# Performance work log

Measured on AMD Instinct MI355X. Metric: run time of the kernel, lower is better.

## Reference

```python
import jax, jax.numpy as jnp
from jax import lax
import numpy as np

B, N, C = 16, 4096, 64
RATIO = 0.25
M = int(N * RATIO)      # 1024 sampled centers
R = 0.2                 # radius
K = 64                  # max_num_neighbors
H = 128                 # MLP hidden/out width
NEG = -1e30


def setup_inputs() -> dict:
    key = jax.random.key(0)
    k1, k2, k3, k4 = jax.random.split(key, 4)
    pos = jax.random.uniform(k1, (B, N, 3), dtype=jnp.float32)
    x = jax.random.normal(k2, (B, N, C), dtype=jnp.float32)
    W1 = jax.random.normal(k3, (C + 3, H), dtype=jnp.float32) / np.sqrt(C + 3)
    b1 = jnp.zeros((H,), jnp.float32)
    W2 = jax.random.normal(k4, (H, H), dtype=jnp.float32) / np.sqrt(H)
    b2 = jnp.zeros((H,), jnp.float32)
    return {"x": x, "pos": pos, "W1": W1, "b1": b1, "W2": W2, "b2": b2}


def _fps_single(p, m):
    """Farthest point sampling on one cloud p:[N,3] -> m int32 indices (start at 0)."""
    n = p.shape[0]
    big = jnp.full((n,), jnp.finfo(p.dtype).max, dtype=p.dtype)

    def step(carry, _):
        dists, last = carry
        d = jnp.sum((p - p[last]) ** 2, axis=-1)       # [N]
        dists = jnp.minimum(dists, d)
        nxt = jnp.argmax(dists).astype(jnp.int32)
        return (dists, nxt), nxt

    (_, _), idxs = lax.scan(step, (big, jnp.int32(0)), None, length=m - 1)
    return jnp.concatenate([jnp.zeros((1,), jnp.int32), idxs])


def reference(x, pos, W1, b1, W2, b2):
    # --- FPS: sample M centers per cloud ---
    idx = jax.vmap(lambda p: _fps_single(p, M))(pos)                 # [B,M] int32
    pos_s = jax.vmap(lambda p, i: p[i])(pos, idx)                    # [B,M,3]

    # --- radius ball query: pairwise sq-dists via |a|^2+|b|^2-2ab (no [B,M,N,3]) ---
    pn = jnp.sum(pos * pos, axis=-1)                                 # [B,N]
    sn = jnp.sum(pos_s * pos_s, axis=-1)                             # [B,M]
    d2 = sn[:, :, None] + pn[:, None, :] - 2.0 * jnp.einsum("bmc,bnc->bmn", pos_s, pos)
    mask = d2 <= R * R                                               # [B,M,N]

    # first K in-radius neighbors by index (torch_cluster-style capped neighbor list)
    ar = jnp.arange(N, dtype=jnp.int32)
    scored = jnp.where(mask, -ar[None, None, :], -N)                 # valid -> -idx
    vals, _ = lax.top_k(scored, K)                                   # [B,M,K]
    nbr = -vals                                                      # neighbor indices, N = invalid
    valid = nbr < N                                                  # [B,M,K]
    nbr_c = jnp.minimum(nbr, N - 1)

    # --- gather -> MLP -> masked max aggregation (PointConv, aggr='max') ---
    x_j = jax.vmap(lambda xb, ib: xb[ib])(x, nbr_c)                  # [B,M,K,C]
    pos_j = jax.vmap(lambda pb, ib: pb[ib])(pos, nbr_c)              # [B,M,K,3]
    feat = jnp.concatenate([x_j, pos_j - pos_s[:, :, None, :]], axis=-1)  # [B,M,K,C+3]

    h = jax.nn.relu(jnp.einsum("bmkc,ch->bmkh", feat, W1) + b1)
    h = jax.nn.relu(jnp.einsum("bmkh,hg->bmkg", h, W2) + b2)          # [B,M,K,H]

    h = jnp.where(valid[..., None], h, NEG)
    out = jnp.max(h, axis=2)                                          # [B,M,H]
    out = jnp.where(jnp.any(valid, axis=2)[..., None], out, 0.0)
    return out, pos_s
```

## Files before the change

kernel.cpp:

```cpp
#include <hip/hip_runtime.h>
#include <cstdint>
#include <cstddef>

#define BB 16
#define NN 4096
#define CC 64
#define MM 1024
#define KK 64
#define HH 128
#define NEGV -1.0e30f

#define FTH 256
#define FPT 16
#define NPROD 16
#define GTOT 256
#define PSTRIDE 32

#define KC1 96
#define SA 104
#define SH 136
#define HSTRIDE 41984

typedef __attribute__((ext_vector_type(8))) short bf16x8;
typedef __attribute__((ext_vector_type(4))) float f32x4;
typedef __attribute__((ext_vector_type(2))) float f32x2;

__device__ __forceinline__ unsigned int f2bf(float f) {
  unsigned int u = __float_as_uint(f);
  return (u + 0x7fffu + ((u >> 16) & 1u)) >> 16;
}
__device__ __forceinline__ void split2(float f, unsigned int& h, unsigned int& l) {
  h = f2bf(f);
  float hf = __uint_as_float(h << 16);
  l = f2bf(f - hf);
}

template <int CTRL, int RM>
__device__ __forceinline__ void dpp_max64(unsigned int& hi, unsigned int& lo) {
  unsigned int shi = (unsigned int)__builtin_amdgcn_update_dpp(
      (int)hi, (int)hi, CTRL, RM, 0xf, false);
  unsigned int slo = (unsigned int)__builtin_amdgcn_update_dpp(
      (int)lo, (int)lo, CTRL, RM, 0xf, false);
  unsigned long long cur = ((unsigned long long)hi << 32) | lo;
  unsigned long long oth = ((unsigned long long)shi << 32) | slo;
  if (oth > cur) { hi = shi; lo = slo; }
}

__global__ __launch_bounds__(256) void pn_kernel(const float* __restrict__ pos,
                                                 float* __restrict__ pn) {
#pragma clang fp contract(off)
  int i = blockIdx.x * 256 + threadIdx.x;
  if (i < BB * NN) {
    float x = pos[(size_t)i * 3 + 0];
    float y = pos[(size_t)i * 3 + 1];
    float z = pos[(size_t)i * 3 + 2];
    pn[i] = (x * x + y * y) + z * z;
  }
}

__global__ __launch_bounds__(128) void wprep_kernel(
    const float* __restrict__ W1, const float* __restrict__ W2,
    unsigned short* __restrict__ W1Th, unsigned short* __restrict__ W1Tl,
    unsigned short* __restrict__ W2Th, unsigned short* __restrict__ W2Tl) {
  const int n = blockIdx.x, t = threadIdx.x;
  if (t < KC1) {
    float v = (t < 67) ? W1[(size_t)t * HH + n] : 0.0f;
    unsigned int h, l; split2(v, h, l);
    W1Th[n * KC1 + t] = (unsigned short)h;
    W1Tl[n * KC1 + t] = (unsigned short)l;
  }
  {
    float v = W2[(size_t)t * HH + n];
    unsigned int h, l; split2(v, h, l);
    W2Th[n * HH + t] = (unsigned short)h;
    W2Tl[n * HH + t] = (unsigned short)l;
  }
}

__global__ void init_kernel(unsigned int* progress, unsigned int* claim) {
  int t = threadIdx.x;
  if (t < NPROD * PSTRIDE) progress[t] = 0u;
  if (t == NPROD * PSTRIDE) *claim = 0u;
}

__global__ __launch_bounds__(512, 2) void fused_kernel(
    const float* __restrict__ pos, const float* __restrict__ x,
    const float* __restrict__ pn,
    float* __restrict__ pos_s_ws, float* __restrict__ pos_s_out,
    const unsigned short* __restrict__ W1Th, const unsigned short* __restrict__ W1Tl,
    const unsigned short* __restrict__ W2Th, const unsigned short* __restrict__ W2Tl,
    const float* __restrict__ b1, const float* __restrict__ b2,
    float* __restrict__ out,
    unsigned int* __restrict__ progress, unsigned int* __restrict__ claim) {
#pragma clang fp contract(off)
  __shared__ __attribute__((aligned(16))) unsigned char LBUF[83968];
  const int t = threadIdx.x;
  const int lane = t & 63;

  if (blockIdx.x < NPROD) {
    if (t >= FTH) return;
    __builtin_amdgcn_s_setprio(3);
    const int wv = t >> 6;
    const int b = blockIdx.x;
    float4* P4 = (float4*)LBUF;
    float* SXa = (float*)(LBUF + 65536);
    float* SYa = (float*)(LBUF + 69632);
    float* SZa = (float*)(LBUF + 73728);
    unsigned long long* cand = (unsigned long long*)(LBUF + 77824);
    const float* pb = pos + (size_t)b * NN * 3;
    f32x2 px[8], py[8], pz[8], dd[8];
#pragma unroll
    for (int j = 0; j < FPT; ++j) {
      int i = t + j * FTH;
      float xx = pb[i * 3 + 0], yy = pb[i * 3 + 1], zz = pb[i * 3 + 2];
      P4[i] = make_float4(xx, yy, zz, 0.0f);
      px[j >> 1][j & 1] = xx;
      py[j >> 1][j & 1] = yy;
      pz[j >> 1][j & 1] = zz;
      dd[j >> 1][j & 1] = 3.4028234663852886e38f;
    }
    __syncthreads();
    float4 c4 = P4[0];
    float sx = c4.x, sy = c4.y, sz = c4.z;
    if (t == 0) { SXa[0] = sx; SYa[0] = sy; SZa[0] = sz; }

    for (int m = 1; m < MM; ++m) {
      float bv = -1.0f;
      int   bi = 0;
      f32x2 s2x = {sx, sx}, s2y = {sy, sy}, s2z = {sz, sz};
#pragma unroll
      for (int k = 0; k < 8; ++k) {
        f32x2 dx = px[k] - s2x, dy = py[k] - s2y, dz = pz[k] - s2z;
        f32x2 d2 = (dx * dx + dy * dy) + dz * dz;
        float n0 = fminf(dd[k][0], d2[0]);
        float n1 = fminf(dd[k][1], d2[1]);
        dd[k][0] = n0;
        dd[k][1] = n1;
        if (n0 > bv) { bv = n0; bi = t + ((2 * k) << 8); }
        if (n1 > bv) { bv = n1; bi = t + ((2 * k + 1) << 8); }
      }
      unsigned int kh = __float_as_uint(bv);
      unsigned int kl = ~(unsigned int)bi;
      dpp_max64<0x111, 0xf>(kh, kl);
      dpp_max64<0x112, 0xf>(kh, kl);
      dpp_max64<0x114, 0xf>(kh, kl);
      dpp_max64<0x118, 0xf>(kh, kl);
      dpp_max64<0x142, 0xa>(kh, kl);
      dpp_max64<0x143, 0xc>(kh, kl);
      if (lane == 63)
        cand[(m & 1) * 4 + wv] = ((unsigned long long)kh << 32) | kl;
      __syncthreads();
      unsigned long long best = cand[(m & 1) * 4 + 0];
#pragma unroll
      for (int w = 1; w < 4; ++w) {
        unsigned long long ok = cand[(m & 1) * 4 + w];
        best = ok > best ? ok : best;
      }
      int fi = (int)(~(unsigned int)(best & 0xffffffffull));
      float4 w4 = P4[fi];
      sx = w4.x; sy = w4.y; sz = w4.z;
      if (t == 0) {
        SXa[m] = sx; SYa[m] = sy; SZa[m] = sz;
        if ((m & 15) == 15) {
          int base = m - 15;
          for (int j = 0; j < 16; ++j) {
            size_t o = ((size_t)b * MM + base + j) * 3;
            __hip_atomic_store(&pos_s_ws[o + 0], SXa[base + j], __ATOMIC_RELAXED, __HIP_MEMORY_SCOPE_AGENT);
            __hip_atomic_store(&pos_s_ws[o + 1], SYa[base + j], __ATOMIC_RELAXED, __HIP_MEMORY_SCOPE_AGENT);
            __hip_atomic_store(&pos_s_ws[o + 2], SZa[base + j], __ATOMIC_RELAXED, __HIP_MEMORY_SCOPE_AGENT);
          }
        } else if ((m & 15) == 0) {
          asm volatile("s_waitcnt vmcnt(0)" ::: "memory");
          __hip_atomic_store(&progress[b * PSTRIDE], (unsigned int)m,
                             __ATOMIC_RELAXED, __HIP_MEMORY_SCOPE_AGENT);
        }
      }
    }
    __syncthreads();
    if (t == 0) {
      asm volatile("s_waitcnt vmcnt(0)" ::: "memory");
      __hip_atomic_store(&progress[b * PSTRIDE], (unsigned int)MM,
                         __ATOMIC_RELAXED, __HIP_MEMORY_SCOPE_AGENT);
    }
    for (int i = t; i < MM; i += FTH) {
      size_t o = ((size_t)b * MM + i) * 3;
      pos_s_out[o + 0] = SXa[i];
      pos_s_out[o + 1] = SYa[i];
      pos_s_out[o + 2] = SZa[i];
    }
    return;
  }

  const int h = t >> 8;
  const int th = t & 255;
  const int wvh = (t >> 6) & 3;
  unsigned char* HB = LBUF + h * HSTRIDE;
  unsigned short* Ah = (unsigned short*)HB;
  unsigned short* Al = (unsigned short*)(HB + 64 * SA * 2);
  unsigned short* Hh = (unsigned short*)HB;
  unsigned short* Hl = (unsigned short*)(HB + 64 * SH * 2);
  int* nbr_s = (int*)(HB + 34816);
  unsigned long long* masksL = (unsigned long long*)(HB + 35072);
  int* prefixL = (int*)(HB + 35584);
  float* ctr = (float*)(HB + 35840);
  int* cntS = (int*)(HB + 35856);
  volatile int* cidShare = (int*)(LBUF + 83960);
  const int r = lane & 15, q = lane >> 4;
  const int wbase = wvh * 32;

  while (true) {
    if (t == 0) {
      unsigned int i = __hip_atomic_fetch_add(claim, 2u, __ATOMIC_RELAXED,
                                              __HIP_MEMORY_SCOPE_AGENT);
      *cidShare = (int)i;
    }
    __syncthreads();
    int i0 = *cidShare;
    if (i0 >= BB * MM) break;
    const int i = i0 + h;
    const bool active = (i < BB * MM);
    const int cid = active ? (((i & 15) << 10) | (i >> 4)) : 0;
    const int b = cid >> 10;
    const int m = cid & 1023;

    if (active && th < 64) {
      while ((int)__hip_atomic_load(&progress[b * PSTRIDE], __ATOMIC_RELAXED,
                                    __HIP_MEMORY_SCOPE_AGENT) <= m)
        __builtin_amdgcn_s_sleep(64);
    }
    if (active && th < 3)
      ctr[th] = __hip_atomic_load(&pos_s_ws[(size_t)cid * 3 + th],
                                  __ATOMIC_RELAXED, __HIP_MEMORY_SCOPE_AGENT);
    __syncthreads();

    const float sx = ctr[0], sy = ctr[1], sz = ctr[2];
    const float sn = (sx * sx + sy * sy) + sz * sz;
    const float* pb = pos + (size_t)b * NN * 3;
    const float* pnb = pn + (size_t)b * NN;
    if (active) {
#pragma unroll
      for (int cc = 0; cc < 16; ++cc) {
        int c = (wvh << 4) + cc;
        int n = (c << 6) + lane;
        float xx = pb[n * 3 + 0], yy = pb[n * 3 + 1], zz = pb[n * 3 + 2];
        float dot = __builtin_fmaf(sz, zz, __builtin_fmaf(sy, yy, sx * xx));
        float d2 = (sn + pnb[n]) - 2.0f * dot;
        bool pred = d2 <= 0.04f;
        unsigned long long mask = __ballot(pred);
        if (lane == 0) masksL[c] = mask;
      }
    }
    __syncthreads();
    if (active && th < 64) {
      int pc = (int)__popcll(masksL[lane]);
      int incl = pc;
#pragma unroll
      for (int off = 1; off < 64; off <<= 1) {
        int o2 = __shfl_up(incl, off, 64);
        if (lane >= off) incl += o2;
      }
      prefixL[lane] = incl - pc;
      if (lane == 63) *cntS = incl < KK ? incl : KK;
    }
    __syncthreads();
    const int cnt = *cntS;
    if (active) {
#pragma unroll
      for (int cc = 0; cc < 16; ++cc) {
        int c = (wvh << 4) + cc;
        unsigned long long mk = masksL[c];
        bool pred = (mk >> lane) & 1ull;
        int slot = prefixL[c] + (int)__popcll(mk & ((1ull << lane) - 1ull));
        if (pred && slot < KK) nbr_s[slot] = (c << 6) + lane;
      }
    }
    __syncthreads();

    if (active) {
      const int kn = th >> 2, p = th & 3;
      float vals[16];
      float d0 = 0.0f, d1 = 0.0f, d2v = 0.0f;
      if (kn < cnt) {
        int n = nbr_s[kn];
        const float* xp = x + ((size_t)b * NN + n) * CC + p * 16;
#pragma unroll
        for (int ii = 0; ii < 4; ++ii) {
          float4 v = ((const float4*)xp)[ii];
          vals[ii * 4 + 0] = v.x; vals[ii * 4 + 1] = v.y;
          vals[ii * 4 + 2] = v.z; vals[ii * 4 + 3] = v.w;
        }
        if (p == 0) {
          const float* pp = pos + ((size_t)b * NN + n) * 3;
          d0 = pp[0] - sx; d1 = pp[1] - sy; d2v = pp[2] - sz;
        }
      } else {
#pragma unroll
        for (int ii = 0; ii < 16; ++ii) vals[ii] = 0.0f;
      }
#pragma unroll
      for (int j = 0; j < 16; j += 2) {
        unsigned int h0, l0, h1, l1;
        split2(vals[j], h0, l0);
        split2(vals[j + 1], h1, l1);
        int c = p * 16 + j;
        *(unsigned int*)&Ah[kn * SA + c] = h0 | (h1 << 16);
        *(unsigned int*)&Al[kn * SA + c] = l0 | (l1 << 16);
      }
      if (p == 0) {
        unsigned int h0, l0, h1, l1, h2, l2;
        split2(d0, h0, l0); split2(d1, h1, l1); split2(d2v, h2, l2);
        *(unsigned int*)&Ah[kn * SA + 64] = h0 | (h1 << 16);
        *(unsigned int*)&Al[kn * SA + 64] = l0 | (l1 << 16);
        *(unsigned int*)&Ah[kn * SA + 66] = h2;
        *(unsigned int*)&Al[kn * SA + 66] = l2;
      } else if (p == 1) {
#pragma unroll
        for (int c = 68; c < 80; c += 2) {
          *(unsigned int*)&Ah[kn * SA + c] = 0u;
          *(unsigned int*)&Al[kn * SA + c] = 0u;
        }
      } else if (p == 2) {
#pragma unroll
        for (int c = 80; c < 96; c += 2) {
          *(unsigned int*)&Ah[kn * SA + c] = 0u;
          *(unsigned int*)&Al[kn * SA + c] = 0u;
        }
      }
    }
    __syncthreads();

    f32x4 acc[4][2];
#pragma unroll
    for (int mt = 0; mt < 4; ++mt)
#pragma unroll
      for (int nt = 0; nt < 2; ++nt) acc[mt][nt] = (f32x4)0.0f;

    if (active) {
#pragma unroll
      for (int kc = 0; kc < 3; ++kc) {
        bf16x8 bh[2], bl[2];
#pragma unroll
        for (int nt = 0; nt < 2; ++nt) {
          int o = (wbase + nt * 16 + r) * KC1 + kc * 32 + q * 8;
          bh[nt] = *(const bf16x8*)(W1Th + o);
          bl[nt] = *(const bf16x8*)(W1Tl + o);
        }
#pragma unroll
        for (int mt = 0; mt < 4; ++mt) {
          int o = (mt * 16 + r) * SA + kc * 32 + q * 8;
          bf16x8 ah = *(const bf16x8*)&Ah[o];
          bf16x8 al = *(const bf16x8*)&Al[o];
#pragma unroll
          for (int nt = 0; nt < 2; ++nt) {
            acc[mt][nt] = __builtin_amdgcn_mfma_f32_16x16x32_bf16(ah, bh[nt], acc[mt][nt], 0, 0, 0);
            acc[mt][nt] = __builtin_amdgcn_mfma_f32_16x16x32_bf16(al, bh[nt], acc[mt][nt], 0, 0, 0);
            acc[mt][nt] = __builtin_amdgcn_mfma_f32_16x16x32_bf16(ah, bl[nt], acc[mt][nt], 0, 0, 0);
          }
        }
      }
    }
    __syncthreads();

    if (active) {
      float b1v[2] = { b1[wbase + r], b1[wbase + 16 + r] };
#pragma unroll
      for (int mt = 0; mt < 4; ++mt)
#pragma unroll
        for (int nt = 0; nt < 2; ++nt)
#pragma unroll
          for (int ii = 0; ii < 4; ++ii) {
            int mm = mt * 16 + q * 4 + ii;
            int n = wbase + nt * 16 + r;
            float v = fmaxf(acc[mt][nt][ii] + b1v[nt], 0.0f);
            unsigned int hh2, ll2; split2(v, hh2, ll2);
            Hh[mm * SH + n] = (unsigned short)hh2;
            Hl[mm * SH + n] = (unsigned short)ll2;
          }
    }
    __syncthreads();

#pragma unroll
    for (int mt = 0; mt < 4; ++mt)
#pragma unroll
      for (int nt = 0; nt < 2; ++nt) acc[mt][nt] = (f32x4)0.0f;
    if (active) {
#pragma unroll
      for (int kc = 0; kc < 4; ++kc) {
        bf16x8 bh[2], bl[2];
#pragma unroll
        for (int nt = 0; nt < 2; ++nt) {
          int o = (wbase + nt * 16 + r) * HH + kc * 32 + q * 8;
          bh[nt] = *(const bf16x8*)(W2Th + o);
          bl[nt] = *(const bf16x8*)(W2Tl + o);
        }
#pragma unroll
        for (int mt = 0; mt < 4; ++mt) {
          int o = (mt * 16 + r) * SH + kc * 32 + q * 8;
          bf16x8 ah = *(const bf16x8*)&Hh[o];
          bf16x8 al = *(const bf16x8*)&Hl[o];
#pragma unroll
          for (int nt = 0; nt < 2; ++nt) {
            acc[mt][nt] = __builtin_amdgcn_mfma_f32_16x16x32_bf16(ah, bh[nt], acc[mt][nt], 0, 0, 0);
            acc[mt][nt] = __builtin_amdgcn_mfma_f32_16x16x32_bf16(al, bh[nt], acc[mt][nt], 0, 0, 0);
            acc[mt][nt] = __builtin_amdgcn_mfma_f32_16x16x32_bf16(ah, bl[nt], acc[mt][nt], 0, 0, 0);
          }
        }
      }
      float b2v[2] = { b2[wbase + r], b2[wbase + 16 + r] };
#pragma unroll
      for (int nt = 0; nt < 2; ++nt) {
        float vmax = NEGV;
#pragma unroll
        for (int mt = 0; mt < 4; ++mt)
#pragma unroll
          for (int ii = 0; ii < 4; ++ii) {
            int mm = mt * 16 + q * 4 + ii;
            float v = fmaxf(acc[mt][nt][ii] + b2v[nt], 0.0f);
            if (mm < cnt) vmax = fmaxf(vmax, v);
          }
        vmax = fmaxf(vmax, __shfl_xor(vmax, 16, 64));
        vmax = fmaxf(vmax, __shfl_xor(vmax, 32, 64));
        if (q == 0)
          out[(size_t)cid * HH + wbase + nt * 16 + r] = (cnt > 0) ? vmax : 0.0f;
      }
    }
    __syncthreads();
  }
}

extern "C" void kernel_launch(void* const* d_in, const int* in_sizes, int n_in,
                              void* d_out, int out_size, void* d_ws, size_t ws_size,
                              hipStream_t stream) {
  const float* x   = (const float*)d_in[0];
  const float* pos = (const float*)d_in[1];
  const float* W1  = (const float*)d_in[2];
  const float* b1  = (const float*)d_in[3];
  const float* W2  = (const float*)d_in[4];
  const float* b2  = (const float*)d_in[5];
  float* out = (float*)d_out;
  float* pos_s_out = out + (size_t)BB * MM * HH;

  char* ws = (char*)d_ws;
  float* pos_s_ws = (float*)(ws);
  float* pn       = (float*)(ws + 196608);
  unsigned short* W1Th = (unsigned short*)(ws + 458752);
  unsigned short* W1Tl = (unsigned short*)(ws + 483328);
  unsigned short* W2Th = (unsigned short*)(ws + 507904);
  unsigned short* W2Tl = (unsigned short*)(ws + 540672);
  unsigned int* progress = (unsigned int*)(ws + 573440);
  unsigned int* claim    = (unsigned int*)(ws + 575488);

  wprep_kernel<<<HH, 128, 0, stream>>>(W1, W2, W1Th, W1Tl, W2Th, W2Tl);
  pn_kernel<<<(BB * NN) / 256, 256, 0, stream>>>(pos, pn);
  init_kernel<<<1, NPROD * PSTRIDE + 64, 0, stream>>>(progress, claim);
  fused_kernel<<<GTOT, 512, 0, stream>>>(pos, x, pn, pos_s_ws, pos_s_out,
                                         W1Th, W1Tl, W2Th, W2Tl, b1, b2, out,
                                         progress, claim);
}
```

Before: 799.2 us.

## Replace FPS per-step barrier with LDS flag spin and tree-reduce local argmax

In the farthest-point-sampling producer blocks, each step's __syncthreads is replaced by versioned LDS slots: lane 63 of each wave writes its key plus the step number as a tag, and every wave spins until all four slots carry the current tag. The per-thread argmax over 16 points also becomes a pairwise tree reduction instead of a serial compare chain, which shortens the dependency chain. The aim is to cut barrier and serial-latency cost on the critical FPS loop. In exchange it relies on LDS write ordering and on the double-buffered slots not being overwritten early, and spinning waves use issue slots.

```diff
diff --git a/kernel.cpp b/kernel.cpp
--- a/kernel.cpp
+++ b/kernel.cpp
@@ -106,7 +106,7 @@
     float* SXa = (float*)(LBUF + 65536);
     float* SYa = (float*)(LBUF + 69632);
     float* SZa = (float*)(LBUF + 73728);
-    unsigned long long* cand = (unsigned long long*)(LBUF + 77824);
+    uint4* slots = (uint4*)(LBUF + 77824);
     const float* pb = pos + (size_t)b * NN * 3;
     f32x2 px[8], py[8], pz[8], dd[8];
 #pragma unroll
@@ -119,15 +119,18 @@
       pz[j >> 1][j & 1] = zz;
       dd[j >> 1][j & 1] = 3.4028234663852886e38f;
     }
+    if (t < 8) {
+      uint4 z4; z4.x = 0u; z4.y = 0u; z4.z = 0u; z4.w = 0u;
+      slots[t] = z4;
+    }
     __syncthreads();
     float4 c4 = P4[0];
     float sx = c4.x, sy = c4.y, sz = c4.z;
     if (t == 0) { SXa[0] = sx; SYa[0] = sy; SZa[0] = sz; }
 
     for (int m = 1; m < MM; ++m) {
-      float bv = -1.0f;
-      int   bi = 0;
       f32x2 s2x = {sx, sx}, s2y = {sy, sy}, s2z = {sz, sz};
+      float nv[16];
 #pragma unroll
       for (int k = 0; k < 8; ++k) {
         f32x2 dx = px[k] - s2x, dy = py[k] - s2y, dz = pz[k] - s2z;
@@ -136,9 +139,35 @@
         float n1 = fminf(dd[k][1], d2[1]);
         dd[k][0] = n0;
         dd[k][1] = n1;
-        if (n0 > bv) { bv = n0; bi = t + ((2 * k) << 8); }
-        if (n1 > bv) { bv = n1; bi = t + ((2 * k + 1) << 8); }
-      }
+        nv[2 * k] = n0;
+        nv[2 * k + 1] = n1;
+      }
+      float tv[8]; int ti[8];
+#pragma unroll
+      for (int k = 0; k < 8; ++k) {
+        bool c = nv[2 * k + 1] > nv[2 * k];
+        tv[k] = c ? nv[2 * k + 1] : nv[2 * k];
+        ti[k] = c ? (2 * k + 1) : (2 * k);
+      }
+      float uv[4]; int ui[4];
+#pragma unroll
+      for (int k = 0; k < 4; ++k) {
+        bool c = tv[2 * k + 1] > tv[2 * k];
+        uv[k] = c ? tv[2 * k + 1] : tv[2 * k];
+        ui[k] = c ? ti[2 * k + 1] : ti[2 * k];
+      }
+      float wv2[2]; int wi2[2];
+#pragma unroll
+      for (int k = 0; k < 2; ++k) {
+        bool c = uv[2 * k + 1] > uv[2 * k];
+        wv2[k] = c ? uv[2 * k + 1] : uv[2 * k];
+        wi2[k] = c ? ui[2 * k + 1] : ui[2 * k];
+      }
+      bool cf = wv2[1] > wv2[0];
+      float bv = cf ? wv2[1] : wv2[0];
+      int bj = cf ? wi2[1] : wi2[0];
+      int bi = t + (bj << 8);
+
       unsigned int kh = __float_as_uint(bv);
       unsigned int kl = ~(unsigned int)bi;
       dpp_max64<0x111, 0xf>(kh, kl);
@@ -147,15 +176,34 @@
       dpp_max64<0x118, 0xf>(kh, kl);
       dpp_max64<0x142, 0xa>(kh, kl);
       dpp_max64<0x143, 0xc>(kh, kl);
-      if (lane == 63)
-        cand[(m & 1) * 4 + wv] = ((unsigned long long)kh << 32) | kl;
-      __syncthreads();
-      unsigned long long best = cand[(m & 1) * 4 + 0];
-#pragma unroll
-      for (int w = 1; w < 4; ++w) {
-        unsigned long long ok = cand[(m & 1) * 4 + w];
-        best = ok > best ? ok : best;
-      }
+      const int p = m & 1;
+      const unsigned int mu = (unsigned int)m;
+      if (lane == 63) {
+        volatile unsigned int* sw = (volatile unsigned int*)&slots[p * 4 + wv];
+        sw[1] = kh;
+        sw[2] = kl;
+        asm volatile("s_waitcnt lgkmcnt(0)" ::: "memory");
+        sw[0] = mu;
+        sw[3] = mu;
+      }
+      uint4 c0, c1, c2, c3;
+      for (;;) {
+        __asm__ __volatile__("" ::: "memory");
+        c0 = slots[p * 4 + 0];
+        c1 = slots[p * 4 + 1];
+        c2 = slots[p * 4 + 2];
+        c3 = slots[p * 4 + 3];
+        if (c0.x == mu && c0.w == mu && c1.x == mu && c1.w == mu &&
+            c2.x == mu && c2.w == mu && c3.x == mu && c3.w == mu)
+          break;
+      }
+      unsigned long long k0 = ((unsigned long long)c0.y << 32) | c0.z;
+      unsigned long long k1 = ((unsigned long long)c1.y << 32) | c1.z;
+      unsigned long long k2 = ((unsigned long long)c2.y << 32) | c2.z;
+      unsigned long long k3 = ((unsigned long long)c3.y << 32) | c3.z;
+      unsigned long long b01 = k0 > k1 ? k0 : k1;
+      unsigned long long b23 = k2 > k3 ? k2 : k3;
+      unsigned long long best = b01 > b23 ? b01 : b23;
       int fi = (int)(~(unsigned int)(best & 0xffffffffull));
       float4 w4 = P4[fi];
       sx = w4.x; sy = w4.y; sz = w4.z;
@@ -171,7 +219,7 @@
           }
         } else if ((m & 15) == 0) {
           asm volatile("s_waitcnt vmcnt(0)" ::: "memory");
-          __hip_atomic_store(&progress[b * PSTRIDE], (unsigned int)m,
+          __hip_atomic_store(&progress[b * PSTRIDE], mu,
                              __ATOMIC_RELAXED, __HIP_MEMORY_SCOPE_AGENT);
         }
       }
```

Result: slower. 1.073 ms (+34.3%).
